# Optimization experiments

Measured on AMD Instinct MI355X. Metric: run time of the kernel, lower is better.

## Reference

```python
import jax, jax.numpy as jnp
import numpy as np

B, Hd, Wd, C, NH, WS = 8, 128, 128, 192, 6, 8
HDIM = int(C * 2.0)   # FFN hidden = 384
RED = C // 8          # AIM channel-gate reduction = 24


def setup_inputs() -> dict:
    key = jax.random.key(0)
    ks = jax.random.split(key, 12)
    s = 0.02
    return {
        "x": jax.random.normal(ks[0], (B, Hd * Wd, C), jnp.float32),
        "H": Hd,
        "W": Wd,
        "n1_w": jnp.ones((C,), jnp.float32),
        "n1_b": jnp.zeros((C,), jnp.float32),
        "qkv_w": jax.random.normal(ks[1], (C, 3 * C), jnp.float32) * s,
        "proj_w": jax.random.normal(ks[2], (C, C), jnp.float32) * s,
        "proj_b": jnp.zeros((C,), jnp.float32),
        "attn_bias": jax.random.normal(ks[3], (NH, WS * WS, WS * WS), jnp.float32) * s,
        "conv_w": jax.random.normal(ks[4], (C, 1, 3, 3), jnp.float32) * s,
        "cg_w1": jax.random.normal(ks[5], (RED, C), jnp.float32) * s,
        "cg_w2": jax.random.normal(ks[6], (C, RED), jnp.float32) * s,
        "n2_w": jnp.ones((C,), jnp.float32),
        "n2_b": jnp.zeros((C,), jnp.float32),
        "fc1_w": jax.random.normal(ks[7], (C, HDIM), jnp.float32) * s,
        "smix_w": jax.random.normal(ks[8], (HDIM, 1, 3, 3), jnp.float32) * s,
        "fc2_w": jax.random.normal(ks[9], (HDIM, C), jnp.float32) * s,
    }


def _ln(x, w, b):
    m = x.mean(-1, keepdims=True)
    v = ((x - m) ** 2).mean(-1, keepdims=True)
    return (x - m) * jax.lax.rsqrt(v + 1e-5) * w + b


def _dwconv(x, w, H, W):
    # x: [B, L, Cx] -> depthwise 3x3 'same' conv -> [B, L, Cx]
    Bx, L, Cx = x.shape
    xi = x.transpose(0, 2, 1).reshape(Bx, Cx, H, W)
    y = jax.lax.conv_general_dilated(
        xi, w, (1, 1), 'SAME', feature_group_count=Cx,
        dimension_numbers=('NCHW', 'OIHW', 'NCHW'))
    return y.reshape(Bx, Cx, L).transpose(0, 2, 1)


def _window_attn(x, H, W, qkv_w, proj_w, proj_b, bias):
    Bx, L, Cx = x.shape
    nHw, nWw = H // WS, W // WS  # H, W are multiples of WS here (no padding needed)
    hd = Cx // NH
    # [B, L, C] -> [B*nH*nW, ws*ws, C]
    xw = (x.reshape(Bx, nHw, WS, nWw, WS, Cx)
           .transpose(0, 1, 3, 2, 4, 5)
           .reshape(Bx * nHw * nWw, WS * WS, Cx))
    qkv = (xw @ qkv_w).reshape(-1, WS * WS, 3, NH, hd).transpose(2, 0, 3, 1, 4)
    q, k, v = qkv[0], qkv[1], qkv[2]          # [Bw, nh, N, hd]
    logits = (q * hd ** -0.5) @ k.transpose(0, 1, 3, 2) + bias[None]
    attn = jax.nn.softmax(logits, axis=-1)
    out = (attn @ v).transpose(0, 2, 1, 3).reshape(-1, WS * WS, Cx)
    out = out @ proj_w + proj_b
    # windows -> [B, L, C]
    return (out.reshape(Bx, nHw, nWw, WS, WS, Cx)
               .transpose(0, 1, 3, 2, 4, 5)
               .reshape(Bx, L, Cx))


def reference(x, H, W, n1_w, n1_b, qkv_w, proj_w, proj_b, attn_bias,
              conv_w, cg_w1, cg_w2, n2_w, n2_b, fc1_w, smix_w, fc2_w):
    n1 = _ln(x, n1_w, n1_b)
    attn_feat = _window_attn(n1, H, W, qkv_w, proj_w, proj_b, attn_bias)
    conv_feat = jax.nn.gelu(_dwconv(n1, conv_w, H, W), approximate=False)
    # AIM: channel_modulates_spatial (btype == 'spatial')
    pooled = conv_feat.mean(axis=1)                                   # [B, C]
    cm = jax.nn.sigmoid(jax.nn.gelu(pooled @ cg_w1.T, approximate=False) @ cg_w2.T)
    x = x + attn_feat * cm[:, None, :] + conv_feat                    # residual (DropPath=id)
    # FFN with depthwise spatial mixing
    n2 = _ln(x, n2_w, n2_b)
    h = jax.nn.gelu(n2 @ fc1_w, approximate=False)                    # [B, L, HDIM]
    h = _dwconv(h, smix_w, H, W)
    return x + h @ fc2_w
```

## Files before the change

### kernel.cpp

```cpp
#include <hip/hip_runtime.h>
#include <hip/hip_bf16.h>
#include <math.h>

#define BATCH 8
#define CCH 192
#define LTOK 16384
#define BL 131072LL
#define NWIN 2048
#define NHEADS 6

typedef __hip_bfloat16 bf16;
typedef __bf16 bfr;
typedef bfr bf16x8 __attribute__((ext_vector_type(8)));
typedef float f32x4 __attribute__((ext_vector_type(4)));
typedef unsigned short u16x8 __attribute__((ext_vector_type(8)));
typedef unsigned short u16x4 __attribute__((ext_vector_type(4)));
typedef unsigned int u32x2 __attribute__((ext_vector_type(2)));

#define FX     0
#define FN1W   1
#define FN1B   2
#define FQKVW  3
#define FPROJW 4
#define FPROJB 5
#define FBIAS  6
#define FCONVW 7
#define FCG1   8
#define FCG2   9
#define FN2W   10
#define FN2B   11
#define FFC1   12
#define FSMIX  13
#define FFC2   14

struct InPtrs { const void* p[15]; int n[15]; };

__device__ __forceinline__ float ldin(const void* p, long long i, int f32) {
    return f32 ? ((const float*)p)[i]
               : __bfloat162float(((const bf16*)p)[i]);
}

__device__ __forceinline__ float bfcvt(unsigned short u) {
    return __uint_as_float((unsigned)u << 16);
}

__device__ __forceinline__ f32x4 ld4f(const void* p, long long i, int f32) {
    if (f32) return *(const f32x4*)((const float*)p + i);
    u16x4 v = *(const u16x4*)((const bf16*)p + i);
    f32x4 r;
    r[0] = bfcvt(v[0]); r[1] = bfcvt(v[1]); r[2] = bfcvt(v[2]); r[3] = bfcvt(v[3]);
    return r;
}
__device__ __forceinline__ f32x4 ld4b(const bf16* p, long long i) {
    u16x4 v = *(const u16x4*)(p + i);
    f32x4 r;
    r[0] = bfcvt(v[0]); r[1] = bfcvt(v[1]); r[2] = bfcvt(v[2]); r[3] = bfcvt(v[3]);
    return r;
}
__device__ __forceinline__ void st4b(bf16* p, long long i, f32x4 v) {
    union { bf16 h; unsigned short u; } cv;
    u16x4 o;
    cv.h = __float2bfloat16(v[0]); o[0] = cv.u;
    cv.h = __float2bfloat16(v[1]); o[1] = cv.u;
    cv.h = __float2bfloat16(v[2]); o[2] = cv.u;
    cv.h = __float2bfloat16(v[3]); o[3] = cv.u;
    *(u16x4*)(p + i) = o;
}

__device__ __forceinline__ unsigned pk2bf(float a, float b) {
    union { bf16 h; unsigned short u; } ca, cb;
    ca.h = __float2bfloat16(a);
    cb.h = __float2bfloat16(b);
    return (unsigned)ca.u | ((unsigned)cb.u << 16);
}

__device__ __forceinline__ float gelu_f(float v) {
    return 0.5f * v * (1.0f + erff(v * 0.70710678118654752f));
}

__global__ void probe_k(InPtrs in, int* flags) {
    __shared__ int s_insane, s_evennz, s_oddnz;
    if (threadIdx.x == 0) { s_insane = 0; s_evennz = 0; s_oddnz = 0; }
    __syncthreads();
    int t = blockIdx.x;
    const bf16* p = (const bf16*)in.p[t];
    int n = in.n[t];
    int m = n < 2048 ? n : 2048;
    bool insane = false, evennz = false, oddnz = false;
    for (int i = threadIdx.x; i < m; i += 256) {
        float v = __bfloat162float(p[i]);
        if (!(fabsf(v) <= 1e9f)) insane = true;
        if (v != 0.0f) { if (i & 1) oddnz = true; else evennz = true; }
    }
    if (insane) s_insane = 1;
    if (evennz) s_evennz = 1;
    if (oddnz)  s_oddnz = 1;
    __syncthreads();
    if (threadIdx.x == 0)
        flags[t] = (s_insane || (!s_evennz && s_oddnz)) ? 1 : 0;
}

__global__ void transpose_k(const void* __restrict__ W, bf16* __restrict__ WT,
                            int K, int N, const int* flag) {
    int f = *flag;
    int idx = blockIdx.x * 256 + threadIdx.x;
    if (idx >= K * N) return;
    int k = idx / N, n = idx % N;
    WT[(long long)n * K + k] = __float2bfloat16(ldin(W, idx, f));
}

__global__ void convw_k(const void* __restrict__ W, float* __restrict__ WT,
                        int CX, const int* flag) {
    int f = *flag;
    int idx = blockIdx.x * 256 + threadIdx.x;
    if (idx >= CX * 9) return;
    int c = idx / 9, t = idx - c * 9;
    WT[t * CX + c] = ldin(W, idx, f);
}

__global__ __launch_bounds__(256)
void ln_kernel(const void* __restrict__ x, const void* __restrict__ w,
               const void* __restrict__ b, bf16* __restrict__ out,
               const int* flags) {
    int fx = flags[FX], fw = flags[FN1W], fb = flags[FN1B];
    int wv = threadIdx.x >> 6, lane = threadIdx.x & 63;
    int gw = lane >> 4, l16 = lane & 15;
    long long t = (long long)blockIdx.x * 16 + wv * 4 + gw;
    long long base = t * CCH;
    f32x4 v[3];
#pragma unroll
    for (int k = 0; k < 3; ++k)
        v[k] = ld4f(x, base + l16 * 4 + 64 * k, fx);
    float s = 0.f;
#pragma unroll
    for (int k = 0; k < 3; ++k) s += v[k][0] + v[k][1] + v[k][2] + v[k][3];
    s += __shfl_xor(s, 1); s += __shfl_xor(s, 2);
    s += __shfl_xor(s, 4); s += __shfl_xor(s, 8);
    float mean = s * (1.0f / 192.0f);
    float vs = 0.f;
#pragma unroll
    for (int k = 0; k < 3; ++k)
#pragma unroll
        for (int j = 0; j < 4; ++j) {
            float d = v[k][j] - mean;
            vs += d * d;
        }
    vs += __shfl_xor(vs, 1); vs += __shfl_xor(vs, 2);
    vs += __shfl_xor(vs, 4); vs += __shfl_xor(vs, 8);
    float rstd = rsqrtf(vs * (1.0f / 192.0f) + 1e-5f);
#pragma unroll
    for (int k = 0; k < 3; ++k) {
        int c0 = l16 * 4 + 64 * k;
        f32x4 wv4 = ld4f(w, c0, fw);
        f32x4 bv4 = ld4f(b, c0, fb);
        f32x4 o;
#pragma unroll
        for (int j = 0; j < 4; ++j)
            o[j] = (v[k][j] - mean) * rstd * wv4[j] + bv4[j];
        st4b(out, base + c0, o);
    }
}

template<int EPI, int KK, int NN, typename CT>
__global__ __launch_bounds__(256)
void gemm2_k(const bf16* __restrict__ A_, const bf16* __restrict__ BT_,
             CT* __restrict__ Cmat, const void* __restrict__ bias,
             const float* __restrict__ res, const int* __restrict__ flags) {
    constexpr int KT = KK / 192;
    constexpr int NC = NN / 64;
    constexpr int NITER = NC * KT;
    constexpr int GSTR = KK * 2;
    __shared__ __align__(16) char Ts[64 * 384];

    const int fb = (EPI == 1) ? flags[FPROJB] : 0;
    const int tid = threadIdx.x;
    const int lane = tid & 63, wv = tid >> 6;
    const int r16 = lane & 15, q = lane >> 4;
    const long long m0 = (long long)blockIdx.x * 64;
    const int swz = (r16 & 7) << 4;

    f32x4 pre[6];
    auto loadB = [&](int itn) {
        int nc2 = itn / KT, kt2 = itn - nc2 * KT;
#pragma unroll
        for (int p = 0; p < 6; ++p) {
            int off = p * 4096 + tid * 16;
            int row = off / 384, col = off - row * 384;
            pre[p] = *(const f32x4*)((const char*)BT_ +
                     (long long)(nc2 * 64 + row) * GSTR + kt2 * 384 + col);
        }
    };
    auto writeT = [&]() {
#pragma unroll
        for (int p = 0; p < 6; ++p) {
            int off = p * 4096 + tid * 16;
            int row = off / 384, col = off - row * 384;
            *(f32x4*)(Ts + row * 384 + (col ^ ((row & 7) << 4))) = pre[p];
        }
    };

    loadB(0);

    bf16x8 afrag[KK / 32];
    const char* Arow = Ts + (wv * 16 + r16) * 384;
    const char* asrc = (const char*)(A_ + m0 * KK);
#pragma unroll
    for (int kt = 0; kt < KT; ++kt) {
#pragma unroll
        for (int p = 0; p < 6; ++p) {
            int off = p * 4096 + tid * 16;
            int row = off / 384, col = off - row * 384;
            *(f32x4*)(Ts + row * 384 + (col ^ ((row & 7) << 4))) =
                *(const f32x4*)(asrc + (long long)row * GSTR + kt * 384 + col);
        }
        __syncthreads();
#pragma unroll
        for (int ks = 0; ks < 6; ++ks)
            afrag[kt * 6 + ks] = *(const bf16x8*)(Arow + ((ks * 64 + q * 16) ^ swz));
        __syncthreads();
    }
    writeT();
    __syncthreads();

    f32x4 acc0, acc1, acc2, acc3;

    for (int it = 0; it < NITER; ++it) {
        const int nc = it / KT, kt = it - nc * KT;
        if (kt == 0) {
            acc0 = f32x4{0.f, 0.f, 0.f, 0.f};
            acc1 = acc0; acc2 = acc0; acc3 = acc0;
        }
        const bool nxt = (it + 1 < NITER);
        if (nxt) loadB(it + 1);
#pragma unroll
        for (int ks = 0; ks < 6; ++ks) {
            bf16x8 a = afrag[kt * 6 + ks];
            const char* bb = Ts + r16 * 384 + ((ks * 64 + q * 16) ^ swz);
            bf16x8 b0 = *(const bf16x8*)(bb);
            bf16x8 b1 = *(const bf16x8*)(bb + 16 * 384);
            bf16x8 b2 = *(const bf16x8*)(bb + 32 * 384);
            bf16x8 b3 = *(const bf16x8*)(bb + 48 * 384);
            acc0 = __builtin_amdgcn_mfma_f32_16x16x32_bf16(a, b0, acc0, 0, 0, 0);
            acc1 = __builtin_amdgcn_mfma_f32_16x16x32_bf16(a, b1, acc1, 0, 0, 0);
            acc2 = __builtin_amdgcn_mfma_f32_16x16x32_bf16(a, b2, acc2, 0, 0, 0);
            acc3 = __builtin_amdgcn_mfma_f32_16x16x32_bf16(a, b3, acc3, 0, 0, 0);
        }
        __syncthreads();
        if (nxt) writeT();
        if (kt == KT - 1) {
            f32x4 accs[4] = {acc0, acc1, acc2, acc3};
#pragma unroll
            for (int j = 0; j < 4; ++j) {
                int col = nc * 64 + j * 16 + r16;
#pragma unroll
                for (int r = 0; r < 4; ++r) {
                    long long row = m0 + wv * 16 + q * 4 + r;
                    float v = accs[j][r];
                    if (EPI == 1) v += ldin(bias, col, fb);
                    if (EPI == 2) v = gelu_f(v);
                    if (EPI == 3) v += res[row * NN + col];
                    Cmat[row * NN + col] = (CT)v;
                }
            }
        }
        if (nxt) __syncthreads();
    }
}

__global__ __launch_bounds__(256)
void attn_mfma_k(const bf16* __restrict__ qkv, const void* __restrict__ bias,
                 bf16* __restrict__ attn_cat, const int* flags) {
    __shared__ __align__(16) bfr Vt[4][32][64];
    __shared__ __align__(16) bfr Pb[4][64][72];

    const int fbias = flags[FBIAS];
    const int wv = threadIdx.x >> 6, lane = threadIdx.x & 63;
    const int pair = blockIdx.x * 4 + wv;
    const int w = pair / 6, h = pair - w * 6;
    const int b = w >> 8, rem = w & 255, wy = rem >> 4, wx = rem & 15;
    const int l15 = lane & 15, quad = lane >> 4;
    const long long tokbase = (long long)b * LTOK + (wy * 8) * 128 + wx * 8;

    long long vt = tokbase + (lane >> 3) * 128 + (lane & 7);
    const bfr* vp = (const bfr*)(qkv + vt * 576 + 384 + h * 32);
    bf16x8 v0 = *(const bf16x8*)(vp);
    bf16x8 v1 = *(const bf16x8*)(vp + 8);
    bf16x8 v2 = *(const bf16x8*)(vp + 16);
    bf16x8 v3 = *(const bf16x8*)(vp + 24);

    bf16x8 aq[4], bk[4];
#pragma unroll
    for (int mt = 0; mt < 4; ++mt) {
        int i0 = mt * 16 + l15;
        long long t = tokbase + (i0 >> 3) * 128 + (i0 & 7);
        const bfr* qp = (const bfr*)(qkv + t * 576 + h * 32 + quad * 8);
        aq[mt] = *(const bf16x8*)qp;
        bk[mt] = *(const bf16x8*)(qp + 192);
    }

#pragma unroll
    for (int j = 0; j < 8; ++j) {
        int sc = lane ^ (j << 3);
        Vt[wv][j][sc]      = v0[j];
        Vt[wv][j + 8][sc]  = v1[j];
        Vt[wv][j + 16][sc] = v2[j];
        Vt[wv][j + 24][sc] = v3[j];
    }

    f32x4 T[4][4];
#pragma unroll
    for (int ti = 0; ti < 4; ++ti)
#pragma unroll
        for (int tj = 0; tj < 4; ++tj) {
            f32x4 z = {0.f, 0.f, 0.f, 0.f};
            T[ti][tj] = __builtin_amdgcn_mfma_f32_16x16x32_bf16(bk[ti], aq[tj], z, 0, 0, 0);
        }

    const float scale = 0.17677669529663689f;
    const long long bias0 = (long long)h * 4096;
#pragma unroll
    for (int tj = 0; tj < 4; ++tj) {
        const long long brow = bias0 + (tj * 16 + l15) * 64 + quad * 4;
        float mloc = -3.0e38f;
#pragma unroll
        for (int ti = 0; ti < 4; ++ti) {
            f32x4 bv4 = ld4f(bias, brow + ti * 16, fbias);
#pragma unroll
            for (int r = 0; r < 4; ++r) {
                float v = T[ti][tj][r] * scale + bv4[r];
                T[ti][tj][r] = v;
                mloc = fmaxf(mloc, v);
            }
        }
        mloc = fmaxf(mloc, __shfl_xor(mloc, 16));
        mloc = fmaxf(mloc, __shfl_xor(mloc, 32));
        float l = 0.f;
#pragma unroll
        for (int ti = 0; ti < 4; ++ti)
#pragma unroll
            for (int r = 0; r < 4; ++r) {
                float e = __expf(T[ti][tj][r] - mloc);
                T[ti][tj][r] = e;
                l += e;
            }
        l += __shfl_xor(l, 16);
        l += __shfl_xor(l, 32);
        float linv = 1.0f / l;
#pragma unroll
        for (int ti = 0; ti < 4; ++ti) {
            unsigned wlo = pk2bf(T[ti][tj][0] * linv, T[ti][tj][1] * linv);
            unsigned whi = pk2bf(T[ti][tj][2] * linv, T[ti][tj][3] * linv);
            *(u32x2*)&Pb[wv][tj * 16 + l15][ti * 16 + quad * 4] = u32x2{wlo, whi};
        }
    }

    __syncthreads();

    f32x4 O[4][2];
#pragma unroll
    for (int tj = 0; tj < 4; ++tj)
#pragma unroll
        for (int n2 = 0; n2 < 2; ++n2)
            O[tj][n2] = f32x4{0.f, 0.f, 0.f, 0.f};
    const int vsw = (l15 & 7) << 3;
#pragma unroll
    for (int kc = 0; kc < 2; ++kc) {
        bf16x8 bv0 = *(const bf16x8*)&Vt[wv][l15][(kc * 32 + quad * 8) ^ vsw];
        bf16x8 bv1 = *(const bf16x8*)&Vt[wv][16 + l15][(kc * 32 + quad * 8) ^ vsw];
#pragma unroll
        for (int tj = 0; tj < 4; ++tj) {
            bf16x8 ap = *(const bf16x8*)&Pb[wv][tj * 16 + l15][kc * 32 + quad * 8];
            O[tj][0] = __builtin_amdgcn_mfma_f32_16x16x32_bf16(ap, bv0, O[tj][0], 0, 0, 0);
            O[tj][1] = __builtin_amdgcn_mfma_f32_16x16x32_bf16(ap, bv1, O[tj][1], 0, 0, 0);
        }
    }

#pragma unroll
    for (int tj = 0; tj < 4; ++tj)
#pragma unroll
        for (int n2 = 0; n2 < 2; ++n2)
#pragma unroll
            for (int r = 0; r < 4; ++r) {
                long long row = (long long)w * 64 + tj * 16 + quad * 4 + r;
                attn_cat[row * CCH + h * 32 + n2 * 16 + l15] =
                    __float2bfloat16(O[tj][n2][r]);
            }
}

template<bool GELU, int CX>
__global__ __launch_bounds__(256)
void dwconv_s4_k(const bf16* __restrict__ in, const float* __restrict__ wt,
                 bf16* __restrict__ out) {
    constexpr int CG = CX / 8;
    int cpx = gridDim.x >> 3;
    int lb = (blockIdx.x & 7) * cpx + (blockIdx.x >> 3);
    long long idx = (long long)lb * 256 + threadIdx.x;
    if (idx >= (BL / 4) * CG) return;
    int cg = (int)(idx % CG);
    long long s = idx / CG;
    int xs = (int)(s & 31);
    long long by = s >> 5;
    int y = (int)(by & 127);
    int x0 = xs * 4;
    int c0 = cg * 8;
    const long long rowpix = by * 128;

    float acc[4][8] = {};
#pragma unroll
    for (int dy = -1; dy <= 1; ++dy) {
        int yy = y + dy;
        if (yy < 0 || yy > 127) continue;
        const bf16* rp = in + ((rowpix + dy * 128) + x0) * CX + c0;
        float fcol[6][8];
#pragma unroll
        for (int ci = 0; ci < 6; ++ci) {
            int xx = x0 + ci - 1;
            if (xx < 0 || xx > 127) {
#pragma unroll
                for (int j = 0; j < 8; ++j) fcol[ci][j] = 0.f;
            } else {
                u16x8 v = *(const u16x8*)(rp + (ci - 1) * CX);
#pragma unroll
                for (int j = 0; j < 8; ++j) fcol[ci][j] = bfcvt(v[j]);
            }
        }
        const float* wb = wt + (dy + 1) * 3 * CX + c0;
#pragma unroll
        for (int dx = 0; dx < 3; ++dx) {
            f32x4 w0 = *(const f32x4*)(wb + dx * CX);
            f32x4 w1 = *(const f32x4*)(wb + dx * CX + 4);
#pragma unroll
            for (int px = 0; px < 4; ++px) {
#pragma unroll
                for (int j = 0; j < 4; ++j) {
                    acc[px][j]     += fcol[px + dx][j]     * w0[j];
                    acc[px][j + 4] += fcol[px + dx][j + 4] * w1[j];
                }
            }
        }
    }
#pragma unroll
    for (int px = 0; px < 4; ++px) {
        __attribute__((aligned(16))) unsigned short ob[8];
#pragma unroll
        for (int j = 0; j < 8; ++j) {
            float vv = acc[px][j];
            if (GELU) vv = gelu_f(vv);
            union { bf16 h; unsigned short u; } cv;
            cv.h = __float2bfloat16(vv);
            ob[j] = cv.u;
        }
        *(u16x8*)(out + (rowpix + x0 + px) * CX + c0) = *(const u16x8*)ob;
    }
}

__global__ __launch_bounds__(192)
void pool_k(const bf16* __restrict__ conv, float* __restrict__ pooled) {
    __shared__ float red[8][192];
    int b = blockIdx.x, chunk = blockIdx.y;
    int cg = threadIdx.x % 24, rr = threadIdx.x / 24;
    float acc[8] = {0.f, 0.f, 0.f, 0.f, 0.f, 0.f, 0.f, 0.f};
    long long rowbase = (long long)b * LTOK + chunk * 256;
    for (int r = rr; r < 256; r += 8) {
        u16x8 v = *(const u16x8*)(conv + (rowbase + r) * CCH + cg * 8);
#pragma unroll
        for (int j = 0; j < 8; ++j) acc[j] += bfcvt(v[j]);
    }
#pragma unroll
    for (int j = 0; j < 8; ++j) red[rr][cg * 8 + j] = acc[j];
    __syncthreads();
    if (rr == 0) {
#pragma unroll
        for (int j = 0; j < 8; ++j) {
            float s = 0.f;
#pragma unroll
            for (int i = 0; i < 8; ++i) s += red[i][cg * 8 + j];
            atomicAdd(&pooled[b * CCH + cg * 8 + j], s);
        }
    }
}

__global__ void cm_k(const float* __restrict__ pooled, const void* __restrict__ w1,
                     const void* __restrict__ w2, float* __restrict__ cm,
                     const int* flags) {
    __shared__ float ps[192], g[24];
    int f1 = flags[FCG1], f2 = flags[FCG2];
    int b = blockIdx.x, c = threadIdx.x;
    ps[c] = pooled[b * CCH + c] * (1.0f / 16384.0f);
    __syncthreads();
    if (c < 24) {
        float t = 0.f;
        for (int k = 0; k < 192; ++k) t += ps[k] * ldin(w1, c * 192 + k, f1);
        g[c] = gelu_f(t);
    }
    __syncthreads();
    float s = 0.f;
#pragma unroll
    for (int r = 0; r < 24; ++r) s += g[r] * ldin(w2, c * 24 + r, f2);
    cm[b * CCH + c] = 1.0f / (1.0f + expf(-s));
}

__global__ __launch_bounds__(256)
void x2ln2_k(const void* __restrict__ x, const bf16* __restrict__ attnf,
             const bf16* __restrict__ conv, const float* __restrict__ cm,
             const void* __restrict__ w, const void* __restrict__ bb,
             float* __restrict__ x2, bf16* __restrict__ n2, const int* flags) {
    int fx = flags[FX], fw = flags[FN2W], fb = flags[FN2B];
    int wv = threadIdx.x >> 6, lane = threadIdx.x & 63;
    int gw = lane >> 4, l16 = lane & 15;
    long long t = (long long)blockIdx.x * 16 + wv * 4 + gw;
    int b = (int)(t >> 14);
    int l = (int)(t & 16383);
    int y = l >> 7, xx = l & 127;
    long long wrow = ((long long)b * 256 + (y >> 3) * 16 + (xx >> 3)) * 64 + (y & 7) * 8 + (xx & 7);

    f32x4 sv[3];
#pragma unroll
    for (int k = 0; k < 3; ++k) {
        int c0 = l16 * 4 + 64 * k;
        f32x4 xv  = ld4f(x, t * CCH + c0, fx);
        f32x4 af  = ld4b(attnf, wrow * CCH + c0);
        f32x4 cf  = ld4b(conv, t * CCH + c0);
        f32x4 cmv = *(const f32x4*)(cm + b * CCH + c0);
        f32x4 o;
#pragma unroll
        for (int j = 0; j < 4; ++j)
            o[j] = xv[j] + af[j] * cmv[j] + cf[j];
        *(f32x4*)(x2 + t * CCH + c0) = o;
        sv[k] = o;
    }
    float s = 0.f;
#pragma unroll
    for (int k = 0; k < 3; ++k) s += sv[k][0] + sv[k][1] + sv[k][2] + sv[k][3];
    s += __shfl_xor(s, 1); s += __shfl_xor(s, 2);
    s += __shfl_xor(s, 4); s += __shfl_xor(s, 8);
    float mean = s * (1.0f / 192.0f);
    float vs = 0.f;
#pragma unroll
    for (int k = 0; k < 3; ++k)
#pragma unroll
        for (int j = 0; j < 4; ++j) {
            float d = sv[k][j] - mean;
            vs += d * d;
        }
    vs += __shfl_xor(vs, 1); vs += __shfl_xor(vs, 2);
    vs += __shfl_xor(vs, 4); vs += __shfl_xor(vs, 8);
    float rstd = rsqrtf(vs * (1.0f / 192.0f) + 1e-5f);
#pragma unroll
    for (int k = 0; k < 3; ++k) {
        int c0 = l16 * 4 + 64 * k;
        f32x4 wv4 = ld4f(w, c0, fw);
        f32x4 bv4 = ld4f(bb, c0, fb);
        f32x4 o;
#pragma unroll
        for (int j = 0; j < 4; ++j)
            o[j] = (sv[k][j] - mean) * rstd * wv4[j] + bv4[j];
        st4b(n2, t * CCH + c0, o);
    }
}

extern "C" void kernel_launch(void* const* d_in, const int* in_sizes, int n_in,
                              void* d_out, int out_size, void* d_ws, size_t ws_size,
                              hipStream_t stream) {
    (void)n_in; (void)out_size; (void)ws_size;
    float* out = (float*)d_out;

    char* wsp = (char*)d_ws;
    size_t off = 0;
    auto alloc = [&](size_t bytes) -> char* {
        char* p = wsp + off;
        off += (bytes + 255) & ~(size_t)255;
        return p;
    };
    int*  flags   = (int*)alloc(15 * 4);
    bf16* qkv_wT  = (bf16*)alloc(576 * 192 * 2);
    bf16* proj_wT = (bf16*)alloc(192 * 192 * 2);
    bf16* fc1_wT  = (bf16*)alloc(384 * 192 * 2);
    bf16* fc2_wT  = (bf16*)alloc(192 * 384 * 2);
    float* convwT = (float*)alloc(9 * CCH * 4);
    float* smixwT = (float*)alloc(9 * 384 * 4);
    float* pooled = (float*)alloc(BATCH * CCH * 4);
    float* cm     = (float*)alloc(BATCH * CCH * 4);
    char* Rbig    = alloc(BL * 576 * 2);
    char* Rpair   = alloc(BL * 384 * 2);

    bf16* qkvb  = (bf16*)Rbig;
    bf16* hbuf  = (bf16*)Rbig;
    bf16* attnf = (bf16*)(Rbig + (size_t)BL * 384 * 2);
    bf16* n1    = (bf16*)Rpair;
    bf16* cat   = (bf16*)(Rpair + (size_t)BL * 192 * 2);
    bf16* n2    = n1;
    bf16* convf = cat;
    bf16* h2    = (bf16*)Rpair;
    float* x2   = out;

    const int imap[15] = {0, 3, 4, 5, 6, 7, 8, 9, 10, 11, 12, 13, 14, 15, 16};
    InPtrs ip;
    for (int i = 0; i < 15; ++i) { ip.p[i] = d_in[imap[i]]; ip.n[i] = in_sizes[imap[i]]; }
    const void* x        = d_in[0];
    const void* qkv_w    = d_in[5];
    const void* proj_w   = d_in[6];
    const void* proj_b   = d_in[7];
    const void* attnbias = d_in[8];
    const void* conv_w   = d_in[9];
    const void* cg_w1    = d_in[10];
    const void* cg_w2    = d_in[11];
    const void* fc1_w    = d_in[14];
    const void* smix_w   = d_in[15];
    const void* fc2_w    = d_in[16];

    probe_k<<<15, 256, 0, stream>>>(ip, flags);

    transpose_k<<<(192 * 576 + 255) / 256, 256, 0, stream>>>(qkv_w, qkv_wT, 192, 576, flags + FQKVW);
    transpose_k<<<(192 * 192 + 255) / 256, 256, 0, stream>>>(proj_w, proj_wT, 192, 192, flags + FPROJW);
    transpose_k<<<(192 * 384 + 255) / 256, 256, 0, stream>>>(fc1_w, fc1_wT, 192, 384, flags + FFC1);
    transpose_k<<<(384 * 192 + 255) / 256, 256, 0, stream>>>(fc2_w, fc2_wT, 384, 192, flags + FFC2);
    convw_k<<<(CCH * 9 + 255) / 256, 256, 0, stream>>>(conv_w, convwT, CCH, flags + FCONVW);
    convw_k<<<(384 * 9 + 255) / 256, 256, 0, stream>>>(smix_w, smixwT, 384, flags + FSMIX);
    hipMemsetAsync(pooled, 0, BATCH * CCH * 4, stream);

    ln_kernel<<<BL / 16, 256, 0, stream>>>(x, d_in[3], d_in[4], n1, flags);
    gemm2_k<0, 192, 576, bf16><<<BL / 64, 256, 0, stream>>>(n1, qkv_wT, qkvb, nullptr, nullptr, flags);
    attn_mfma_k<<<NWIN * NHEADS / 4, 256, 0, stream>>>(qkvb, attnbias, cat, flags);
    gemm2_k<1, 192, 192, bf16><<<BL / 64, 256, 0, stream>>>(cat, proj_wT, attnf, proj_b, nullptr, flags);
    dwconv_s4_k<true, 192><<<(int)(BL / 4 * 24 / 256), 256, 0, stream>>>(n1, convwT, convf);
    pool_k<<<dim3(BATCH, 64), 192, 0, stream>>>(convf, pooled);
    cm_k<<<BATCH, 192, 0, stream>>>(pooled, cg_w1, cg_w2, cm, flags);
    x2ln2_k<<<BL / 16, 256, 0, stream>>>(x, attnf, convf, cm, d_in[12], d_in[13], x2, n2, flags);
    gemm2_k<2, 192, 384, bf16><<<BL / 64, 256, 0, stream>>>(n2, fc1_wT, hbuf, nullptr, nullptr, flags);
    dwconv_s4_k<false, 384><<<(int)(BL / 4 * 48 / 256), 256, 0, stream>>>(hbuf, smixwT, h2);
    gemm2_k<3, 384, 192, float><<<BL / 64, 256, 0, stream>>>(h2, fc2_wT, out, nullptr, x2, flags);
}
```

Baseline: 621.4 us.

## Double-buffer B tiles in GEMM LDS and prefetch residual values

The GEMM kernel now uses two LDS buffers. The next B tile is written into the idle buffer while MFMAs read the current one, which removes one __syncthreads per iteration and one per A-fragment load step. In the EPI==3 path, the residual values are loaded into registers at the start of each output column chunk rather than in the epilogue, to hide global load latency. In exchange, the kernel's LDS use doubles to 48KB and register use grows, which may lower occupancy.

```diff
diff --git a/kernel.cpp b/kernel.cpp
--- a/kernel.cpp
+++ b/kernel.cpp
@@ -170,7 +170,7 @@
     constexpr int NC = NN / 64;
     constexpr int NITER = NC * KT;
     constexpr int GSTR = KK * 2;
-    __shared__ __align__(16) char Ts[64 * 384];
+    __shared__ __align__(16) char Ts[2][64 * 384];
 
     const int fb = (EPI == 1) ? flags[FPROJB] : 0;
     const int tid = threadIdx.x;
@@ -190,52 +190,63 @@
                      (long long)(nc2 * 64 + row) * GSTR + kt2 * 384 + col);
         }
     };
-    auto writeT = [&]() {
+    auto writeT = [&](char* buf) {
 #pragma unroll
         for (int p = 0; p < 6; ++p) {
             int off = p * 4096 + tid * 16;
             int row = off / 384, col = off - row * 384;
-            *(f32x4*)(Ts + row * 384 + (col ^ ((row & 7) << 4))) = pre[p];
+            *(f32x4*)(buf + row * 384 + (col ^ ((row & 7) << 4))) = pre[p];
         }
     };
 
     loadB(0);
 
     bf16x8 afrag[KK / 32];
-    const char* Arow = Ts + (wv * 16 + r16) * 384;
     const char* asrc = (const char*)(A_ + m0 * KK);
 #pragma unroll
     for (int kt = 0; kt < KT; ++kt) {
+        char* buf = Ts[kt & 1];
 #pragma unroll
         for (int p = 0; p < 6; ++p) {
             int off = p * 4096 + tid * 16;
             int row = off / 384, col = off - row * 384;
-            *(f32x4*)(Ts + row * 384 + (col ^ ((row & 7) << 4))) =
+            *(f32x4*)(buf + row * 384 + (col ^ ((row & 7) << 4))) =
                 *(const f32x4*)(asrc + (long long)row * GSTR + kt * 384 + col);
         }
         __syncthreads();
+        const char* Arow = buf + (wv * 16 + r16) * 384;
 #pragma unroll
         for (int ks = 0; ks < 6; ++ks)
             afrag[kt * 6 + ks] = *(const bf16x8*)(Arow + ((ks * 64 + q * 16) ^ swz));
-        __syncthreads();
-    }
-    writeT();
+    }
+    int cur = KT & 1;
+    writeT(Ts[cur]);
     __syncthreads();
 
     f32x4 acc0, acc1, acc2, acc3;
+    float resv[16];
 
     for (int it = 0; it < NITER; ++it) {
         const int nc = it / KT, kt = it - nc * KT;
         if (kt == 0) {
             acc0 = f32x4{0.f, 0.f, 0.f, 0.f};
             acc1 = acc0; acc2 = acc0; acc3 = acc0;
+            if (EPI == 3) {
+#pragma unroll
+                for (int j = 0; j < 4; ++j)
+#pragma unroll
+                    for (int r = 0; r < 4; ++r)
+                        resv[j * 4 + r] =
+                            res[(m0 + wv * 16 + q * 4 + r) * NN + nc * 64 + j * 16 + r16];
+            }
         }
         const bool nxt = (it + 1 < NITER);
         if (nxt) loadB(it + 1);
+        const char* bbase = Ts[cur] + r16 * 384;
 #pragma unroll
         for (int ks = 0; ks < 6; ++ks) {
             bf16x8 a = afrag[kt * 6 + ks];
-            const char* bb = Ts + r16 * 384 + ((ks * 64 + q * 16) ^ swz);
+            const char* bb = bbase + ((ks * 64 + q * 16) ^ swz);
             bf16x8 b0 = *(const bf16x8*)(bb);
             bf16x8 b1 = *(const bf16x8*)(bb + 16 * 384);
             bf16x8 b2 = *(const bf16x8*)(bb + 32 * 384);
@@ -245,8 +256,7 @@
             acc2 = __builtin_amdgcn_mfma_f32_16x16x32_bf16(a, b2, acc2, 0, 0, 0);
             acc3 = __builtin_amdgcn_mfma_f32_16x16x32_bf16(a, b3, acc3, 0, 0, 0);
         }
-        __syncthreads();
-        if (nxt) writeT();
+        if (nxt) writeT(Ts[cur ^ 1]);
         if (kt == KT - 1) {
             f32x4 accs[4] = {acc0, acc1, acc2, acc3};
 #pragma unroll
@@ -258,12 +268,13 @@
                     float v = accs[j][r];
                     if (EPI == 1) v += ldin(bias, col, fb);
                     if (EPI == 2) v = gelu_f(v);
-                    if (EPI == 3) v += res[row * NN + col];
+                    if (EPI == 3) v += resv[j * 4 + r];
                     Cmat[row * NN + col] = (CT)v;
                 }
             }
         }
         if (nxt) __syncthreads();
+        cur ^= 1;
     }
 }
 
```

Result: slower. 634.2 us (+2.1%).

## Fuse output projection into window attention kernel; prefetch residual in fc2 epilogue

Applied to the files above, without the earlier changes.

The attention kernel now runs one block per window with six waves, one per head. Each wave writes its head output into shared memory, and the block then applies the 192x192 output projection plus bias with MFMA before writing attnf. This removes the separate proj GEMM launch and the round trip of the concatenated attention tensor through global memory, and buffers are remapped to match. The fc2 GEMM epilogue also loads its residual values into registers at the start of each output column tile, so that load overlaps with the MFMA loop; the cost is extra register pressure and larger shared memory per block.

```diff
diff --git a/kernel.cpp b/kernel.cpp
--- a/kernel.cpp
+++ b/kernel.cpp
@@ -223,12 +223,21 @@
     __syncthreads();
 
     f32x4 acc0, acc1, acc2, acc3;
+    float resv[16];
 
     for (int it = 0; it < NITER; ++it) {
         const int nc = it / KT, kt = it - nc * KT;
         if (kt == 0) {
             acc0 = f32x4{0.f, 0.f, 0.f, 0.f};
             acc1 = acc0; acc2 = acc0; acc3 = acc0;
+            if (EPI == 3) {
+#pragma unroll
+                for (int j = 0; j < 4; ++j)
+#pragma unroll
+                    for (int r = 0; r < 4; ++r)
+                        resv[j * 4 + r] =
+                            res[(m0 + wv * 16 + q * 4 + r) * NN + nc * 64 + j * 16 + r16];
+            }
         }
         const bool nxt = (it + 1 < NITER);
         if (nxt) loadB(it + 1);
@@ -258,7 +267,7 @@
                     float v = accs[j][r];
                     if (EPI == 1) v += ldin(bias, col, fb);
                     if (EPI == 2) v = gelu_f(v);
-                    if (EPI == 3) v += res[row * NN + col];
+                    if (EPI == 3) v += resv[j * 4 + r];
                     Cmat[row * NN + col] = (CT)v;
                 }
             }
@@ -267,19 +276,21 @@
     }
 }
 
-__global__ __launch_bounds__(256)
-void attn_mfma_k(const bf16* __restrict__ qkv, const void* __restrict__ bias,
-                 bf16* __restrict__ attn_cat, const int* flags) {
-    __shared__ __align__(16) bfr Vt[4][32][64];
-    __shared__ __align__(16) bfr Pb[4][64][72];
+__global__ __launch_bounds__(384)
+void attn_proj_k(const bf16* __restrict__ qkv, const void* __restrict__ bias,
+                 const bf16* __restrict__ pwT, const void* __restrict__ proj_b,
+                 bf16* __restrict__ attnf, const int* __restrict__ flags) {
+    __shared__ __align__(16) bfr Vt[6][32][64];
+    __shared__ __align__(16) char PbRaw[6 * 64 * 144];
 
     const int fbias = flags[FBIAS];
-    const int wv = threadIdx.x >> 6, lane = threadIdx.x & 63;
-    const int pair = blockIdx.x * 4 + wv;
-    const int w = pair / 6, h = pair - w * 6;
+    const int h = threadIdx.x >> 6, lane = threadIdx.x & 63;
+    const int w = blockIdx.x;
     const int b = w >> 8, rem = w & 255, wy = rem >> 4, wx = rem & 15;
     const int l15 = lane & 15, quad = lane >> 4;
     const long long tokbase = (long long)b * LTOK + (wy * 8) * 128 + wx * 8;
+
+    bfr (*Pb)[72] = (bfr(*)[72])(PbRaw + h * 64 * 144);
 
     long long vt = tokbase + (lane >> 3) * 128 + (lane & 7);
     const bfr* vp = (const bfr*)(qkv + vt * 576 + 384 + h * 32);
@@ -301,10 +312,10 @@
 #pragma unroll
     for (int j = 0; j < 8; ++j) {
         int sc = lane ^ (j << 3);
-        Vt[wv][j][sc]      = v0[j];
-        Vt[wv][j + 8][sc]  = v1[j];
-        Vt[wv][j + 16][sc] = v2[j];
-        Vt[wv][j + 24][sc] = v3[j];
+        Vt[h][j][sc]      = v0[j];
+        Vt[h][j + 8][sc]  = v1[j];
+        Vt[h][j + 16][sc] = v2[j];
+        Vt[h][j + 24][sc] = v3[j];
     }
 
     f32x4 T[4][4];
@@ -350,7 +361,7 @@
         for (int ti = 0; ti < 4; ++ti) {
             unsigned wlo = pk2bf(T[ti][tj][0] * linv, T[ti][tj][1] * linv);
             unsigned whi = pk2bf(T[ti][tj][2] * linv, T[ti][tj][3] * linv);
-            *(u32x2*)&Pb[wv][tj * 16 + l15][ti * 16 + quad * 4] = u32x2{wlo, whi};
+            *(u32x2*)&Pb[tj * 16 + l15][ti * 16 + quad * 4] = u32x2{wlo, whi};
         }
     }
 
@@ -365,26 +376,65 @@
     const int vsw = (l15 & 7) << 3;
 #pragma unroll
     for (int kc = 0; kc < 2; ++kc) {
-        bf16x8 bv0 = *(const bf16x8*)&Vt[wv][l15][(kc * 32 + quad * 8) ^ vsw];
-        bf16x8 bv1 = *(const bf16x8*)&Vt[wv][16 + l15][(kc * 32 + quad * 8) ^ vsw];
+        bf16x8 bv0 = *(const bf16x8*)&Vt[h][l15][(kc * 32 + quad * 8) ^ vsw];
+        bf16x8 bv1 = *(const bf16x8*)&Vt[h][16 + l15][(kc * 32 + quad * 8) ^ vsw];
 #pragma unroll
         for (int tj = 0; tj < 4; ++tj) {
-            bf16x8 ap = *(const bf16x8*)&Pb[wv][tj * 16 + l15][kc * 32 + quad * 8];
+            bf16x8 ap = *(const bf16x8*)&Pb[tj * 16 + l15][kc * 32 + quad * 8];
             O[tj][0] = __builtin_amdgcn_mfma_f32_16x16x32_bf16(ap, bv0, O[tj][0], 0, 0, 0);
             O[tj][1] = __builtin_amdgcn_mfma_f32_16x16x32_bf16(ap, bv1, O[tj][1], 0, 0, 0);
         }
     }
 
+    __syncthreads();
+
+    bf16* cat = (bf16*)PbRaw;
 #pragma unroll
     for (int tj = 0; tj < 4; ++tj)
 #pragma unroll
         for (int n2 = 0; n2 < 2; ++n2)
 #pragma unroll
+            for (int r = 0; r < 4; ++r)
+                cat[(tj * 16 + quad * 4 + r) * 200 + h * 32 + n2 * 16 + l15] =
+                    __float2bfloat16(O[tj][n2][r]);
+
+    __syncthreads();
+
+    const int fpb = flags[FPROJB];
+    f32x4 pacc[4][2];
+#pragma unroll
+    for (int mt = 0; mt < 4; ++mt) {
+        pacc[mt][0] = f32x4{0.f, 0.f, 0.f, 0.f};
+        pacc[mt][1] = pacc[mt][0];
+    }
+#pragma unroll
+    for (int ks = 0; ks < 6; ++ks) {
+        bf16x8 af[4];
+#pragma unroll
+        for (int mt = 0; mt < 4; ++mt)
+            af[mt] = *(const bf16x8*)&cat[(mt * 16 + l15) * 200 + ks * 32 + quad * 8];
+#pragma unroll
+        for (int nt = 0; nt < 2; ++nt) {
+            int col = h * 32 + nt * 16 + l15;
+            bf16x8 bfr8 = *(const bf16x8*)((const bfr*)pwT + (long long)col * 192 + ks * 32 + quad * 8);
+#pragma unroll
+            for (int mt = 0; mt < 4; ++mt)
+                pacc[mt][nt] = __builtin_amdgcn_mfma_f32_16x16x32_bf16(af[mt], bfr8, pacc[mt][nt], 0, 0, 0);
+        }
+    }
+
+#pragma unroll
+    for (int nt = 0; nt < 2; ++nt) {
+        int col = h * 32 + nt * 16 + l15;
+        float bv = ldin(proj_b, col, fpb);
+#pragma unroll
+        for (int mt = 0; mt < 4; ++mt)
+#pragma unroll
             for (int r = 0; r < 4; ++r) {
-                long long row = (long long)w * 64 + tj * 16 + quad * 4 + r;
-                attn_cat[row * CCH + h * 32 + n2 * 16 + l15] =
-                    __float2bfloat16(O[tj][n2][r]);
+                long long row = (long long)w * 64 + mt * 16 + quad * 4 + r;
+                attnf[row * CCH + col] = __float2bfloat16(pacc[mt][nt][r] + bv);
             }
+    }
 }
 
 template<bool GELU, int CX>
@@ -585,12 +635,11 @@
     char* Rpair   = alloc(BL * 384 * 2);
 
     bf16* qkvb  = (bf16*)Rbig;
+    bf16* convf = (bf16*)Rbig;
     bf16* hbuf  = (bf16*)Rbig;
-    bf16* attnf = (bf16*)(Rbig + (size_t)BL * 384 * 2);
     bf16* n1    = (bf16*)Rpair;
-    bf16* cat   = (bf16*)(Rpair + (size_t)BL * 192 * 2);
+    bf16* attnf = (bf16*)(Rpair + (size_t)BL * 192 * 2);
     bf16* n2    = n1;
-    bf16* convf = cat;
     bf16* h2    = (bf16*)Rpair;
     float* x2   = out;
 
@@ -621,8 +670,7 @@
 
     ln_kernel<<<BL / 16, 256, 0, stream>>>(x, d_in[3], d_in[4], n1, flags);
     gemm2_k<0, 192, 576, bf16><<<BL / 64, 256, 0, stream>>>(n1, qkv_wT, qkvb, nullptr, nullptr, flags);
-    attn_mfma_k<<<NWIN * NHEADS / 4, 256, 0, stream>>>(qkvb, attnbias, cat, flags);
-    gemm2_k<1, 192, 192, bf16><<<BL / 64, 256, 0, stream>>>(cat, proj_wT, attnf, proj_b, nullptr, flags);
+    attn_proj_k<<<NWIN, 384, 0, stream>>>(qkvb, attnbias, proj_wT, proj_b, attnf, flags);
     dwconv_s4_k<true, 192><<<(int)(BL / 4 * 24 / 256), 256, 0, stream>>>(n1, convwT, convf);
     pool_k<<<dim3(BATCH, 64), 192, 0, stream>>>(convf, pooled);
     cm_k<<<BATCH, 192, 0, stream>>>(pooled, cg_w1, cg_w2, cm, flags);
```

After: 618.6 us. No clear change (-0.5%).
